# Performance work log

Measured on AMD Instinct MI355X. Metric: run time of the kernel, lower is better.

## Reference

```python
import jax, jax.numpy as jnp
import numpy as np

# Module config (matches init_kwargs)
RADIUS = 1
N_POINTS = 8
NUM_BINS = 8
DENSITY = True
LBP_MAX = 2 ** N_POINTS - 1  # 255


def _circle_offsets(radius, n_points):
    # skimage local_binary_pattern sampling coordinates:
    # rr = -radius*sin(2*pi*i/P), cc = radius*cos(2*pi*i/P)
    offs = []
    for i in range(n_points):
        ang = 2.0 * np.pi * i / n_points
        dy = -radius * np.sin(ang)
        dx = radius * np.cos(ang)
        # skimage snaps near-integer coords to exact integers (eps rounding)
        if abs(dy - round(dy)) < 1e-8:
            dy = float(round(dy))
        if abs(dx - round(dx)) < 1e-8:
            dx = float(round(dx))
        offs.append((dy, dx))
    return offs


def _bilinear_shift(xp, pad, dy, dx, H, W):
    # Bilinear sample of every pixel's neighbor at constant offset (dy, dx),
    # zero padding outside the image (skimage uses constant-0 border mode).
    fy, fx = int(np.floor(dy)), int(np.floor(dx))
    ty, tx = dy - fy, dx - fx

    def sl(oy, ox):
        return xp[..., pad + oy:pad + oy + H, pad + ox:pad + ox + W]

    return ((1.0 - ty) * (1.0 - tx) * sl(fy, fx)
            + (1.0 - ty) * tx * sl(fy, fx + 1)
            + ty * (1.0 - tx) * sl(fy + 1, fx)
            + ty * tx * sl(fy + 1, fx + 1))


def _lbp_codes(x):
    # x: (B, C, H, W) -> integer-valued LBP codes (B, C, H, W), method='default'
    B, C, H, W = x.shape
    pad = int(np.ceil(RADIUS)) + 1
    xp = jnp.pad(x, ((0, 0), (0, 0), (pad, pad), (pad, pad)))
    code = jnp.zeros(x.shape, dtype=jnp.float32)
    for i, (dy, dx) in enumerate(_circle_offsets(RADIUS, N_POINTS)):
        nb = _bilinear_shift(xp, pad, dy, dx, H, W)
        bit = (nb - x >= 0).astype(jnp.float32)
        code = code + bit * float(2 ** i)
    return code


def _histogram(codes):
    # np.histogram(bins=NUM_BINS, range=(0, LBP_MAX), density=True) per channel
    B, C, H, W = codes.shape
    width = LBP_MAX / NUM_BINS
    idx = jnp.clip((codes * (1.0 / width)).astype(jnp.int32), 0, NUM_BINS - 1)
    idx_flat = idx.reshape(B * C, H * W)
    counts = jax.vmap(
        lambda ix: jnp.zeros((NUM_BINS,), jnp.float32).at[ix].add(1.0)
    )(idx_flat)  # (B*C, NUM_BINS)
    if DENSITY:
        counts = counts / (float(H * W) * width)
    return counts.reshape(B, C, NUM_BINS)


def setup_inputs() -> dict:
    key = jax.random.key(0)
    x = jax.random.normal(key, (32, 3, 512, 512), dtype=jnp.float32)
    return {"x": x}


def reference(x):
    codes = _lbp_codes(x)               # (B, C, H, W)
    hist = _histogram(codes)            # (B, C, NUM_BINS)
    return hist.reshape(hist.shape[0], -1).astype(jnp.float32)  # (B, C*NUM_BINS)
```

## Files before the change

kernel.cpp:

```cpp
#include <hip/hip_runtime.h>

#define W 512
#define H 512
#define CH_PIX (W * H)

__device__ __forceinline__ float2 lr_for(float4 v, float hk, int half, int lane) {
    const float up = __shfl_up(v.w, 1, 64);
    const float dn = __shfl_down(v.x, 1, 64);
    const float eL = half ? hk : 0.0f;
    const float eR = half ? 0.0f : hk;
    float2 r;
    r.x = (lane == 0)  ? eL : up;
    r.y = (lane == 63) ? eR : dn;
    return r;
}

__global__ __launch_bounds__(256) void lbp_main_k(const float* __restrict__ x,
                                                  unsigned int* __restrict__ ws) {
    const int chan = blockIdx.x;
    const int band = blockIdx.y;
    const int tid  = threadIdx.x;
    const int wave  = tid >> 6;
    const int lane  = tid & 63;
    const int strip = wave >> 1;
    const int half  = wave & 1;

    __shared__ unsigned int h[8 * 64];
    for (int i = tid; i < 512; i += 256) h[i] = 0u;
    __syncthreads();

    constexpr double Sd = 0.7071067811865476;
    constexpr double Td = 1.0 - Sd;
    const float wSS = (float)(Sd * Sd);
    const float wST = (float)(Sd * Td);
    const float wTT = (float)(Td * Td);

    const int colbase = half * 256 + (lane << 2);
    const int haloCol = half ? 255 : 256;
    const int cb   = chan * CH_PIX;
    const int y0   = band * 32 + strip * 16;
    const bool lastStrip = (y0 == 496);
    const float* rp = x + cb + y0 * W + colbase;

    unsigned long long c64 = 0ull;

    float4 buf[9];
    #pragma unroll
    for (int k = 0; k < 9; ++k) buf[k] = *(const float4*)(rp + k * W);

    float hvAll = 0.0f;
    {
        int yy = y0 + lane;
        yy = yy > 511 ? 511 : yy;
        if (lane < 17) hvAll = x[cb + yy * W + haloCol];
    }

    auto rowpix = [&](const float4& m4, float mL, float mR,
                      const float4& d4, float dL, float dR) {
        const float cs[4]  = {m4.x, m4.y, m4.z, m4.w};
        const float es[4]  = {m4.y, m4.z, m4.w, mR};
        const float wsA[4] = {mL,   m4.x, m4.y, m4.z};
        const float ss[4]  = {d4.x, d4.y, d4.z, d4.w};
        const float sws[4] = {dL,   d4.x, d4.y, d4.z};
        const float ses[4] = {d4.y, d4.z, d4.w, dR};
        #pragma unroll
        for (int i = 0; i < 4; ++i) {
            const float c  = cs[i];
            const float tc = wTT * c;
            const float ts = wST * ss[i];
            const float nb5 = ((wST * wsA[i] + tc) + wSS * sws[i]) + ts;
            const float nb7 = ((tc + wST * es[i]) + ts) + wSS * ses[i];
            const bool p0 = (nb5   >= c);
            const bool p1 = (ss[i] >= c);
            const bool p2 = (nb7   >= c);
            unsigned int t = p0 ? 0x100u : 1u;
            t = p1 ? (t << 16) : t;
            c64 += (unsigned long long)t << (p2 ? 32 : 0);
        }
    };

    float4 m4  = buf[0];
    float2 mlr = lr_for(m4, __shfl(hvAll, 0, 64), half, lane);
    #pragma unroll
    for (int k = 0; k < 8; ++k) {
        const float4 d4  = buf[k + 1];
        const float2 dlr = lr_for(d4, __shfl(hvAll, k + 1, 64), half, lane);
        rowpix(m4, mlr.x, mlr.y, d4, dlr.x, dlr.y);
        m4 = d4; mlr = dlr;
    }

    #pragma unroll
    for (int k = 0; k < 8; ++k) {
        if (k == 7 && lastStrip) {
            buf[k].x = 0.0f; buf[k].y = 0.0f; buf[k].z = 0.0f; buf[k].w = 0.0f;
        } else {
            buf[k] = *(const float4*)(rp + (9 + k) * W);
        }
    }

    #pragma unroll
    for (int k = 0; k < 8; ++k) {
        const float4 d4 = buf[k];
        const float dhk = (k == 7 && lastStrip) ? 0.0f
                                                : __shfl(hvAll, 9 + k, 64);
        const float2 dlr = lr_for(d4, dhk, half, lane);
        rowpix(m4, mlr.x, mlr.y, d4, dlr.x, dlr.y);
        m4 = d4; mlr = dlr;
    }

    const unsigned int lo = (unsigned int)c64;
    const unsigned int hi = (unsigned int)(c64 >> 32);
    #pragma unroll
    for (int b = 0; b < 4; ++b) {
        atomicAdd(&h[(b       << 6) + lane], (lo >> (b * 8)) & 0xffu);
        atomicAdd(&h[((b + 4) << 6) + lane], (hi >> (b * 8)) & 0xffu);
    }
    __syncthreads();

    unsigned int v0 = h[tid];
    unsigned int v1 = h[tid + 256];
    #pragma unroll
    for (int o = 32; o >= 1; o >>= 1) {
        v0 += __shfl_xor(v0, o, 64);
        v1 += __shfl_xor(v1, o, 64);
    }
    if (lane == 0) {
        unsigned int* dst = &ws[(chan * 16 + band) * 8];
        dst[wave]     = v0;
        dst[wave + 4] = v1;
    }
}

__global__ __launch_bounds__(64) void finalize_k(const unsigned int* __restrict__ ws,
                                                 float* __restrict__ out) {
    const int gid = blockIdx.x * 64 + threadIdx.x;
    if (gid < 768) {
        const int chan = gid >> 3, bin = gid & 7;
        unsigned int s = 0;
        #pragma unroll
        for (int b = 0; b < 16; ++b) s += ws[(chan * 16 + b) * 8 + bin];
        out[gid] = (float)s / 8355840.0f;
    }
}

extern "C" void kernel_launch(void* const* d_in, const int* in_sizes, int n_in,
                              void* d_out, int out_size, void* d_ws, size_t ws_size,
                              hipStream_t stream) {
    const float* x = (const float*)d_in[0];
    unsigned int* wsp = (unsigned int*)d_ws;
    float* out = (float*)d_out;

    dim3 grid(96, 16);
    lbp_main_k<<<grid, 256, 0, stream>>>(x, wsp);
    finalize_k<<<12, 64, 0, stream>>>(wsp, out);
}
```

Measured before the change: 28.14 us.

## Assign full row width per wave with 8 columns per lane

Each wave now covers an entire 512-wide row strip, each lane handling 8 columns via two float4 loads, rather than two waves splitting the row in half. This drops the per-wave halo column load and its shuffles, and halves the grid to 96x8 blocks so each block covers 64 rows. Register use roughly doubles for the row buffers, and with half as many blocks there is less parallelism to hide memory latency.

```diff
diff --git a/kernel.cpp b/kernel.cpp
--- a/kernel.cpp
+++ b/kernel.cpp
@@ -4,26 +4,16 @@
 #define H 512
 #define CH_PIX (W * H)
 
-__device__ __forceinline__ float2 lr_for(float4 v, float hk, int half, int lane) {
-    const float up = __shfl_up(v.w, 1, 64);
-    const float dn = __shfl_down(v.x, 1, 64);
-    const float eL = half ? hk : 0.0f;
-    const float eR = half ? 0.0f : hk;
-    float2 r;
-    r.x = (lane == 0)  ? eL : up;
-    r.y = (lane == 63) ? eR : dn;
-    return r;
-}
-
 __global__ __launch_bounds__(256) void lbp_main_k(const float* __restrict__ x,
                                                   unsigned int* __restrict__ ws) {
     const int chan = blockIdx.x;
-    const int band = blockIdx.y;
+    const int bg   = blockIdx.y;
     const int tid  = threadIdx.x;
-    const int wave  = tid >> 6;
-    const int lane  = tid & 63;
-    const int strip = wave >> 1;
-    const int half  = wave & 1;
+    const int wave = tid >> 6;
+    const int lane = tid & 63;
+    const int strip = bg * 4 + wave;
+    const int y0 = strip * 16;
+    const bool lastStrip = (strip == 31);
 
     __shared__ unsigned int h[8 * 64];
     for (int i = tid; i < 512; i += 256) h[i] = 0u;
@@ -35,43 +25,29 @@
     const float wST = (float)(Sd * Td);
     const float wTT = (float)(Td * Td);
 
-    const int colbase = half * 256 + (lane << 2);
-    const int haloCol = half ? 255 : 256;
-    const int cb   = chan * CH_PIX;
-    const int y0   = band * 32 + strip * 16;
-    const bool lastStrip = (y0 == 496);
-    const float* rp = x + cb + y0 * W + colbase;
+    const float* rp = x + chan * CH_PIX + y0 * W + (lane << 3);
+    const bool l0 = (lane == 0), l63 = (lane == 63);
 
     unsigned long long c64 = 0ull;
 
-    float4 buf[9];
+    float4 bufA[9], bufB[9];
     #pragma unroll
-    for (int k = 0; k < 9; ++k) buf[k] = *(const float4*)(rp + k * W);
-
-    float hvAll = 0.0f;
-    {
-        int yy = y0 + lane;
-        yy = yy > 511 ? 511 : yy;
-        if (lane < 17) hvAll = x[cb + yy * W + haloCol];
+    for (int k = 0; k < 9; ++k) {
+        bufA[k] = *(const float4*)(rp + k * W);
+        bufB[k] = *(const float4*)(rp + k * W + 4);
     }
 
-    auto rowpix = [&](const float4& m4, float mL, float mR,
-                      const float4& d4, float dL, float dR) {
-        const float cs[4]  = {m4.x, m4.y, m4.z, m4.w};
-        const float es[4]  = {m4.y, m4.z, m4.w, mR};
-        const float wsA[4] = {mL,   m4.x, m4.y, m4.z};
-        const float ss[4]  = {d4.x, d4.y, d4.z, d4.w};
-        const float sws[4] = {dL,   d4.x, d4.y, d4.z};
-        const float ses[4] = {d4.y, d4.z, d4.w, dR};
+    auto grp = [&](const float c_[4], const float e_[4], const float w_[4],
+                   const float s_[4], const float sw_[4], const float se_[4]) {
         #pragma unroll
         for (int i = 0; i < 4; ++i) {
-            const float c  = cs[i];
+            const float c  = c_[i];
             const float tc = wTT * c;
-            const float ts = wST * ss[i];
-            const float nb5 = ((wST * wsA[i] + tc) + wSS * sws[i]) + ts;
-            const float nb7 = ((tc + wST * es[i]) + ts) + wSS * ses[i];
+            const float ts = wST * s_[i];
+            const float nb5 = ((wST * w_[i] + tc) + wSS * sw_[i]) + ts;
+            const float nb7 = ((tc + wST * e_[i]) + ts) + wSS * se_[i];
             const bool p0 = (nb5   >= c);
-            const bool p1 = (ss[i] >= c);
+            const bool p1 = (s_[i] >= c);
             const bool p2 = (nb7   >= c);
             unsigned int t = p0 ? 0x100u : 1u;
             t = p1 ? (t << 16) : t;
@@ -79,33 +55,64 @@
         }
     };
 
-    float4 m4  = buf[0];
-    float2 mlr = lr_for(m4, __shfl(hvAll, 0, 64), half, lane);
+    auto rowstep = [&](const float4& ma, const float4& mb, float mL, float mR,
+                       const float4& da, const float4& db, float dL, float dR) {
+        {
+            const float cs[4]  = {ma.x, ma.y, ma.z, ma.w};
+            const float es[4]  = {ma.y, ma.z, ma.w, mb.x};
+            const float wsA[4] = {mL,   ma.x, ma.y, ma.z};
+            const float ss[4]  = {da.x, da.y, da.z, da.w};
+            const float sws[4] = {dL,   da.x, da.y, da.z};
+            const float ses[4] = {da.y, da.z, da.w, db.x};
+            grp(cs, es, wsA, ss, sws, ses);
+        }
+        {
+            const float cs[4]  = {mb.x, mb.y, mb.z, mb.w};
+            const float es[4]  = {mb.y, mb.z, mb.w, mR};
+            const float wsA[4] = {ma.w, mb.x, mb.y, mb.z};
+            const float ss[4]  = {db.x, db.y, db.z, db.w};
+            const float sws[4] = {da.w, db.x, db.y, db.z};
+            const float ses[4] = {db.y, db.z, db.w, dR};
+            grp(cs, es, wsA, ss, sws, ses);
+        }
+    };
+
+    auto edges = [&](const float4& a, const float4& b) -> float2 {
+        const float up = __shfl_up(b.w, 1, 64);
+        const float dn = __shfl_down(a.x, 1, 64);
+        float2 r;
+        r.x = l0  ? 0.0f : up;
+        r.y = l63 ? 0.0f : dn;
+        return r;
+    };
+
+    float4 ma = bufA[0], mb = bufB[0];
+    float2 mlr = edges(ma, mb);
     #pragma unroll
     for (int k = 0; k < 8; ++k) {
-        const float4 d4  = buf[k + 1];
-        const float2 dlr = lr_for(d4, __shfl(hvAll, k + 1, 64), half, lane);
-        rowpix(m4, mlr.x, mlr.y, d4, dlr.x, dlr.y);
-        m4 = d4; mlr = dlr;
+        const float4 da = bufA[k + 1], db = bufB[k + 1];
+        const float2 dlr = edges(da, db);
+        rowstep(ma, mb, mlr.x, mlr.y, da, db, dlr.x, dlr.y);
+        ma = da; mb = db; mlr = dlr;
     }
 
     #pragma unroll
     for (int k = 0; k < 8; ++k) {
         if (k == 7 && lastStrip) {
-            buf[k].x = 0.0f; buf[k].y = 0.0f; buf[k].z = 0.0f; buf[k].w = 0.0f;
+            bufA[k] = make_float4(0.0f, 0.0f, 0.0f, 0.0f);
+            bufB[k] = make_float4(0.0f, 0.0f, 0.0f, 0.0f);
         } else {
-            buf[k] = *(const float4*)(rp + (9 + k) * W);
+            bufA[k] = *(const float4*)(rp + (9 + k) * W);
+            bufB[k] = *(const float4*)(rp + (9 + k) * W + 4);
         }
     }
 
     #pragma unroll
     for (int k = 0; k < 8; ++k) {
-        const float4 d4 = buf[k];
-        const float dhk = (k == 7 && lastStrip) ? 0.0f
-                                                : __shfl(hvAll, 9 + k, 64);
-        const float2 dlr = lr_for(d4, dhk, half, lane);
-        rowpix(m4, mlr.x, mlr.y, d4, dlr.x, dlr.y);
-        m4 = d4; mlr = dlr;
+        const float4 da = bufA[k], db = bufB[k];
+        const float2 dlr = edges(da, db);
+        rowstep(ma, mb, mlr.x, mlr.y, da, db, dlr.x, dlr.y);
+        ma = da; mb = db; mlr = dlr;
     }
 
     const unsigned int lo = (unsigned int)c64;
@@ -125,7 +132,7 @@
         v1 += __shfl_xor(v1, o, 64);
     }
     if (lane == 0) {
-        unsigned int* dst = &ws[(chan * 16 + band) * 8];
+        unsigned int* dst = &ws[(chan * 8 + bg) * 8];
         dst[wave]     = v0;
         dst[wave + 4] = v1;
     }
@@ -138,7 +145,7 @@
         const int chan = gid >> 3, bin = gid & 7;
         unsigned int s = 0;
         #pragma unroll
-        for (int b = 0; b < 16; ++b) s += ws[(chan * 16 + b) * 8 + bin];
+        for (int b = 0; b < 8; ++b) s += ws[(chan * 8 + b) * 8 + bin];
         out[gid] = (float)s / 8355840.0f;
     }
 }
@@ -150,7 +157,7 @@
     unsigned int* wsp = (unsigned int*)d_ws;
     float* out = (float*)d_out;
 
-    dim3 grid(96, 16);
+    dim3 grid(96, 8);
     lbp_main_k<<<grid, 256, 0, stream>>>(x, wsp);
     finalize_k<<<12, 64, 0, stream>>>(wsp, out);
 }
```

After: 39.05 us. 1.39x slower.
